# Kernel optimization log

Measured on AMD Instinct MI355X. Metric: run time of the kernel, lower is better.

## Reference

```python
import jax, jax.numpy as jnp
import numpy as np

B, N, K, H = 2, 2048, 48, 128
NIN = 2 * H          # num_in = 2*num_hidden (ProteinMPNN wiring)
FF = 4 * H           # PositionWiseFeedForward hidden
SCALE = 30.0
EPS = 1e-5           # torch LayerNorm default eps


def _ln(x, g, b):
    m = jnp.mean(x, axis=-1, keepdims=True)
    v = jnp.mean((x - m) ** 2, axis=-1, keepdims=True)
    return (x - m) / jnp.sqrt(v + EPS) * g + b


def _gelu(x):
    return jax.nn.gelu(x, approximate=False)  # torch.nn.GELU default (erf)


def _lin(x, W, b):
    return x @ W + b


def setup_inputs() -> dict:
    key = jax.random.key(0)
    ks = jax.random.split(key, 24)
    s = 0.05
    inp = {
        "h_V": jax.random.normal(ks[0], (B, N, H), jnp.float32),
        "h_E": jax.random.normal(ks[1], (B, N, K, H), jnp.float32),
        "E_idx": jax.random.randint(ks[2], (B, N, K), 0, N, jnp.int64),
        "mask_V": jnp.ones((B, N), jnp.float32),
        "mask_attend": jnp.ones((B, N, K), jnp.float32),
        # message MLP (node update): W1 in = H + NIN = 3H
        "W1": jax.random.normal(ks[3], (3 * H, H), jnp.float32) * s,
        "b1": jnp.zeros((H,), jnp.float32),
        "W2": jax.random.normal(ks[4], (H, H), jnp.float32) * s,
        "b2": jnp.zeros((H,), jnp.float32),
        "W3": jax.random.normal(ks[5], (H, H), jnp.float32) * s,
        "b3": jnp.zeros((H,), jnp.float32),
        # PositionWiseFeedForward
        "Wd_in": jax.random.normal(ks[6], (H, FF), jnp.float32) * s,
        "bd_in": jnp.zeros((FF,), jnp.float32),
        "Wd_out": jax.random.normal(ks[7], (FF, H), jnp.float32) * s,
        "bd_out": jnp.zeros((H,), jnp.float32),
        # edge-update MLP: W11 in = H + NIN = 3H
        "W11": jax.random.normal(ks[8], (3 * H, H), jnp.float32) * s,
        "b11": jnp.zeros((H,), jnp.float32),
        "W12": jax.random.normal(ks[9], (H, H), jnp.float32) * s,
        "b12": jnp.zeros((H,), jnp.float32),
        "W13": jax.random.normal(ks[10], (H, H), jnp.float32) * s,
        "b13": jnp.zeros((H,), jnp.float32),
        # LayerNorms
        "n1g": jnp.ones((H,), jnp.float32), "n1b": jnp.zeros((H,), jnp.float32),
        "n2g": jnp.ones((H,), jnp.float32), "n2b": jnp.zeros((H,), jnp.float32),
        "n3g": jnp.ones((H,), jnp.float32), "n3b": jnp.zeros((H,), jnp.float32),
    }
    return inp


def reference(h_V, h_E, E_idx, mask_V, mask_attend,
              W1, b1, W2, b2, W3, b3,
              Wd_in, bd_in, Wd_out, bd_out,
              W11, b11, W12, b12, W13, b13,
              n1g, n1b, n2g, n2b, n3g, n3b):
    gather = jax.vmap(lambda hv, idx: hv[idx])  # [B,N,H],[B,N,K] -> [B,N,K,H]

    # --- node update: cat_neighbors_nodes + expand + 3-layer GELU MLP ---
    h_nb = gather(h_V, E_idx)                                   # [B,N,K,H]
    hV_exp = jnp.broadcast_to(h_V[:, :, None, :], h_nb.shape)   # [B,N,K,H]
    h_EV = jnp.concatenate([hV_exp, h_E, h_nb], axis=-1)        # [B,N,K,3H]
    h_msg = _lin(_gelu(_lin(_gelu(_lin(h_EV, W1, b1)), W2, b2)), W3, b3)
    h_msg = mask_attend[..., None] * h_msg
    dh = jnp.sum(h_msg, axis=-2) / SCALE                        # masked-sum reduce
    h_V = _ln(h_V + dh, n1g, n1b)

    # --- position-wise FFN ---
    dh = _lin(_gelu(_lin(h_V, Wd_in, bd_in)), Wd_out, bd_out)
    h_V = _ln(h_V + dh, n2g, n2b)
    h_V = mask_V[..., None] * h_V

    # --- edge update (not last layer) ---
    h_nb2 = gather(h_V, E_idx)
    hV_exp2 = jnp.broadcast_to(h_V[:, :, None, :], h_nb2.shape)
    h_EV2 = jnp.concatenate([hV_exp2, h_E, h_nb2], axis=-1)     # [B,N,K,3H]
    h_msg2 = _lin(_gelu(_lin(_gelu(_lin(h_EV2, W11, b11)), W12, b12)), W13, b13)
    h_E = _ln(h_E + h_msg2, n3g, n3b)
    return (h_V, h_E)
```

## Files before the change

### kernel.cpp

```cpp
#include <hip/hip_runtime.h>
#include <hip/hip_bf16.h>
#include <stdint.h>

#define XP2 264
#define MP 136
#define FFP 520
#define EPIP 132

typedef __attribute__((ext_vector_type(8))) short bf16x8;
typedef __attribute__((ext_vector_type(4))) float f32x4;

__device__ __forceinline__ f32x4 mfma16(bf16x8 a, bf16x8 b, f32x4 c) {
  return __builtin_amdgcn_mfma_f32_16x16x32_bf16(a, b, c, 0, 0, 0);
}

__device__ __forceinline__ uint16_t f2b(float f) {
  union { __hip_bfloat16 h; uint16_t u; } v;
  v.h = __float2bfloat16(f);
  return v.u;
}
__device__ __forceinline__ uint32_t pk2f(float a, float b) {
  union { __hip_bfloat162 h; uint32_t u; } v;
  v.h = __float22bfloat162_rn(make_float2(a, b));
  return v.u;
}
__device__ __forceinline__ float gelu_f(float x) {
  float u = __builtin_fmaf(x * x, 0.044715f, 1.0f);
  float e = __builtin_amdgcn_exp2f(-2.302585093f * x * u);
  return x * __builtin_amdgcn_rcpf(1.0f + e);
}

__global__ __launch_bounds__(256) void k_prep(
    const float* __restrict__ hV,
    const float* __restrict__ W1, const float* __restrict__ W2, const float* __restrict__ W3,
    const float* __restrict__ WdIn, const float* __restrict__ WdOut,
    const float* __restrict__ W11, const float* __restrict__ W12, const float* __restrict__ W13,
    uint16_t* __restrict__ hVb,
    uint16_t* __restrict__ W1t, uint16_t* __restrict__ W2t, uint16_t* __restrict__ W3t,
    uint16_t* __restrict__ WdInT, uint16_t* __restrict__ WdOutT,
    uint16_t* __restrict__ W11t, uint16_t* __restrict__ W12t, uint16_t* __restrict__ W13t) {
  int i = blockIdx.x * 256 + threadIdx.x;
  if (i < 524288) { hVb[i] = f2b(hV[i]); return; }
  int j = i - 524288;
  if (j < 49152) { int n = j / 384, k = j - n * 384; W1t[j] = f2b(W1[k * 128 + n]); return; }
  j -= 49152;
  if (j < 16384) { int n = j >> 7, k = j & 127; W2t[j] = f2b(W2[k * 128 + n]); return; }
  j -= 16384;
  if (j < 16384) { int n = j >> 7, k = j & 127; W3t[j] = f2b(W3[k * 128 + n]); return; }
  j -= 16384;
  if (j < 65536) { int n = j >> 7, k = j & 127; WdInT[j] = f2b(WdIn[k * 512 + n]); return; }
  j -= 65536;
  if (j < 65536) { int n = j >> 9, k = j & 511; WdOutT[j] = f2b(WdOut[k * 128 + n]); return; }
  j -= 65536;
  if (j < 49152) { int n = j / 384, k = j - n * 384; W11t[j] = f2b(W11[k * 128 + n]); return; }
  j -= 49152;
  if (j < 16384) { int n = j >> 7, k = j & 127; W12t[j] = f2b(W12[k * 128 + n]); return; }
  j -= 16384;
  if (j < 16384) { int n = j >> 7, k = j & 127; W13t[j] = f2b(W13[k * 128 + n]); return; }
}

__global__ __launch_bounds__(256) void k_vec(
    const uint16_t* __restrict__ Xb, const uint16_t* __restrict__ Wt,
    const float* __restrict__ bias, float* __restrict__ C) {
  const int tid = threadIdx.x;
  const int lane = tid & 63, w = tid >> 6, l15 = lane & 15, lg = lane >> 4;
  const int row0 = blockIdx.x * 64 + w * 16;
  f32x4 acc[8] = {};
#pragma unroll
  for (int ks = 0; ks < 4; ++ks) {
    bf16x8 a = *(const bf16x8*)(Xb + (row0 + l15) * 128 + ks * 32 + lg * 8);
#pragma unroll
    for (int j = 0; j < 8; ++j) {
      bf16x8 bb = *(const bf16x8*)(Wt + (j * 16 + l15) * 384 + ks * 32 + lg * 8);
      acc[j] = mfma16(a, bb, acc[j]);
    }
  }
#pragma unroll
  for (int j = 0; j < 8; ++j) {
    float bs = bias[j * 16 + l15];
#pragma unroll
    for (int r = 0; r < 4; ++r)
      C[(row0 + lg * 4 + r) * 128 + j * 16 + l15] = acc[j][r] + bs;
  }
}

#define BUILD_XT(GSRC)                                                              \
  do {                                                                              \
    for (int idx = tid; idx < 48 * 32; idx += 256) {                                \
      int k_ = idx >> 5;                                                            \
      int c_ = idx & 31;                                                            \
      uint4 v_;                                                                     \
      if (c_ < 16) {                                                                \
        const float* s_ = hE + (size_t)(bn * 48 + k_) * 128 + (c_ << 3);            \
        float4 f0_ = *(const float4*)s_;                                            \
        float4 f1_ = *(const float4*)(s_ + 4);                                      \
        v_ = make_uint4(pk2f(f0_.x, f0_.y), pk2f(f0_.z, f0_.w),                     \
                        pk2f(f1_.x, f1_.y), pk2f(f1_.z, f1_.w));                    \
      } else {                                                                      \
        v_ = *(const uint4*)((GSRC) + (size_t)nbr[k_] * 128 + ((c_ - 16) << 3));    \
      }                                                                             \
      *(uint4*)(xt + k_ * XP2 + (c_ << 3)) = v_;                                    \
    }                                                                               \
  } while (0)

#define PRELOAD_W384(WT, WF)                                                        \
  do {                                                                              \
    const uint16_t* p0_ = (WT) + (w * 32 + l15) * 384 + 128 + lg * 8;               \
    const uint16_t* p1_ = p0_ + 16 * 384;                                           \
    _Pragma("unroll") for (int ks = 0; ks < 8; ++ks) {                              \
      WF[ks] = *(const bf16x8*)(p0_ + ks * 32);                                     \
      WF[8 + ks] = *(const bf16x8*)(p1_ + ks * 32);                                 \
    }                                                                               \
  } while (0)

#define PRELOAD_W128(WT, WF)                                                        \
  do {                                                                              \
    const uint16_t* p0_ = (WT) + (w * 32 + l15) * 128 + lg * 8;                     \
    const uint16_t* p1_ = p0_ + 16 * 128;                                           \
    _Pragma("unroll") for (int ks = 0; ks < 4; ++ks) {                              \
      WF[ks] = *(const bf16x8*)(p0_ + ks * 32);                                     \
      WF[4 + ks] = *(const bf16x8*)(p1_ + ks * 32);                                 \
    }                                                                               \
  } while (0)

#define LAYER256R(WF, ACC)                                                          \
  do {                                                                              \
    _Pragma("unroll") for (int ks = 0; ks < 8; ++ks)                                \
    _Pragma("unroll") for (int m = 0; m < 3; ++m) {                                 \
      bf16x8 a_ = *(const bf16x8*)(xt + (m * 16 + l15) * XP2 + ks * 32 + lg * 8);   \
      ACC[m][0] = mfma16(a_, WF[ks], ACC[m][0]);                                    \
      ACC[m][1] = mfma16(a_, WF[8 + ks], ACC[m][1]);                                \
    }                                                                               \
  } while (0)

#define LAYER128R(WF, ASRC, ACC)                                                    \
  do {                                                                              \
    _Pragma("unroll") for (int ks = 0; ks < 4; ++ks)                                \
    _Pragma("unroll") for (int m = 0; m < 3; ++m) {                                 \
      bf16x8 a_ = *(const bf16x8*)((ASRC) + (m * 16 + l15) * MP + ks * 32 + lg * 8);\
      ACC[m][0] = mfma16(a_, WF[ks], ACC[m][0]);                                    \
      ACC[m][1] = mfma16(a_, WF[4 + ks], ACC[m][1]);                                \
    }                                                                               \
  } while (0)

#define GSTORE(ACC, BIAS, DST)                                                      \
  do {                                                                              \
    float bA_ = (BIAS)[w * 32 + l15];                                               \
    float bB_ = (BIAS)[w * 32 + 16 + l15];                                          \
    _Pragma("unroll") for (int m = 0; m < 3; ++m)                                   \
    _Pragma("unroll") for (int r = 0; r < 4; ++r) {                                 \
      int row_ = m * 16 + lg * 4 + r;                                               \
      (DST)[row_ * MP + w * 32 + l15] = f2b(gelu_f(ACC[m][0][r] + bA_));            \
      (DST)[row_ * MP + w * 32 + 16 + l15] = f2b(gelu_f(ACC[m][1][r] + bB_));       \
    }                                                                               \
  } while (0)

#define GSTORE0(ACC, DST)                                                           \
  do {                                                                              \
    _Pragma("unroll") for (int m = 0; m < 3; ++m)                                   \
    _Pragma("unroll") for (int r = 0; r < 4; ++r) {                                 \
      int row_ = m * 16 + lg * 4 + r;                                               \
      (DST)[row_ * MP + w * 32 + l15] = f2b(gelu_f(ACC[m][0][r]));                  \
      (DST)[row_ * MP + w * 32 + 16 + l15] = f2b(gelu_f(ACC[m][1][r]));             \
    }                                                                               \
  } while (0)

#define ACC_INIT(ACC, CV)                                                           \
  do {                                                                              \
    float c0_ = (CV)[bn * 128 + w * 32 + l15];                                      \
    float c1_ = (CV)[bn * 128 + w * 32 + 16 + l15];                                 \
    _Pragma("unroll") for (int m = 0; m < 3; ++m) {                                 \
      ACC[m][0] = (f32x4){c0_, c0_, c0_, c0_};                                      \
      ACC[m][1] = (f32x4){c1_, c1_, c1_, c1_};                                      \
    }                                                                               \
  } while (0)

__global__ __launch_bounds__(256, 4) void k_node(
    const float* __restrict__ hV, const float* __restrict__ hE,
    const int* __restrict__ eidx, const float* __restrict__ maskA,
    const float* __restrict__ bias2, const float* __restrict__ bias3,
    const float* __restrict__ g1, const float* __restrict__ be1,
    const uint16_t* __restrict__ hVb, const float* __restrict__ C1,
    const uint16_t* __restrict__ W1t, const uint16_t* __restrict__ W2t,
    const uint16_t* __restrict__ W3t,
    float* __restrict__ hV1, uint16_t* __restrict__ hV1b) {
  __shared__ __align__(16) unsigned char lds[26880];
  uint16_t* xt = (uint16_t*)lds;
  uint16_t* midA = (uint16_t*)lds;
  uint16_t* midB = (uint16_t*)(lds + 13056);
  int* nbr = (int*)(lds + 26112);
  float* dh = (float*)(lds + 26368);

  const int tid = threadIdx.x;
  const int lane = tid & 63;
  const int w = tid >> 6;
  const int l15 = lane & 15;
  const int lg = lane >> 4;
  const int bn = blockIdx.x;
  const int b = bn >> 11;

  bf16x8 w1f[16];
  PRELOAD_W384(W1t, w1f);

  if (tid < 48) nbr[tid] = (b << 11) + eidx[bn * 48 + tid];
  __syncthreads();

  BUILD_XT(hVb);
  __syncthreads();

  f32x4 acc1[3][2];
  ACC_INIT(acc1, C1);
  LAYER256R(w1f, acc1);
  bf16x8 w2f[8];
  PRELOAD_W128(W2t, w2f);
  __syncthreads();
  GSTORE0(acc1, midA);
  __syncthreads();

  f32x4 acc2[3][2] = {};
  LAYER128R(w2f, midA, acc2);
  bf16x8 w3f[8];
  PRELOAD_W128(W3t, w3f);
  GSTORE(acc2, bias2, midB);
  __syncthreads();

  f32x4 acc3[3][2] = {};
  LAYER128R(w3f, midB, acc3);

  {
    float bA = bias3[w * 32 + l15];
    float bB = bias3[w * 32 + 16 + l15];
    float s0 = 0.f, s1 = 0.f;
#pragma unroll
    for (int m = 0; m < 3; ++m)
#pragma unroll
      for (int r = 0; r < 4; ++r) {
        int row = m * 16 + lg * 4 + r;
        float mk = maskA[bn * 48 + row];
        s0 += (acc3[m][0][r] + bA) * mk;
        s1 += (acc3[m][1][r] + bB) * mk;
      }
    s0 += __shfl_xor(s0, 16); s0 += __shfl_xor(s0, 32);
    s1 += __shfl_xor(s1, 16); s1 += __shfl_xor(s1, 32);
    if (lg == 0) { dh[w * 32 + l15] = s0; dh[w * 32 + 16 + l15] = s1; }
  }
  __syncthreads();

  if (w == 0) {
    const float inv = 1.0f / 30.0f;
    float x0 = hV[bn * 128 + lane] + dh[lane] * inv;
    float x1 = hV[bn * 128 + 64 + lane] + dh[64 + lane] * inv;
    float s = x0 + x1, q = x0 * x0 + x1 * x1;
#pragma unroll
    for (int off = 1; off < 64; off <<= 1) {
      s += __shfl_xor(s, off);
      q += __shfl_xor(q, off);
    }
    float mean = s * (1.0f / 128.0f);
    float var = q * (1.0f / 128.0f) - mean * mean;
    float rstd = rsqrtf(var + 1e-5f);
    float y0 = (x0 - mean) * rstd * g1[lane] + be1[lane];
    float y1 = (x1 - mean) * rstd * g1[64 + lane] + be1[64 + lane];
    hV1[bn * 128 + lane] = y0;
    hV1[bn * 128 + 64 + lane] = y1;
    hV1b[bn * 128 + lane] = f2b(y0);
    hV1b[bn * 128 + 64 + lane] = f2b(y1);
  }
}

__global__ __launch_bounds__(256, 2) void k_ffn(
    const float* __restrict__ hV1, const uint16_t* __restrict__ hV1b,
    const float* __restrict__ maskV,
    const float* __restrict__ bdin, const float* __restrict__ bdout,
    const float* __restrict__ g2, const float* __restrict__ be2,
    const uint16_t* __restrict__ WdInT, const uint16_t* __restrict__ WdOutT,
    float* __restrict__ outV, uint16_t* __restrict__ hV2b) {
  __shared__ __align__(16) unsigned char lds[20992];
  uint16_t* xa = (uint16_t*)lds;
  uint16_t* mf = (uint16_t*)(lds + 4352);
  float* epi = (float*)(lds + 4352);

  const int tid = threadIdx.x;
  const int lane = tid & 63;
  const int w = tid >> 6;
  const int l15 = lane & 15;
  const int lg = lane >> 4;
  const int node0 = blockIdx.x * 16;

  {
    int row = tid >> 4, c = tid & 15;
    *(uint4*)(xa + row * 136 + (c << 3)) =
        *(const uint4*)(hV1b + (node0 + row) * 128 + (c << 3));
  }
  __syncthreads();

  f32x4 acc[8] = {};
  {
    const uint16_t* ar = xa + l15 * 136 + lg * 8;
#pragma unroll
    for (int ks = 0; ks < 4; ++ks) {
      bf16x8 a = *(const bf16x8*)(ar + ks * 32);
#pragma unroll
      for (int j = 0; j < 8; ++j) {
        bf16x8 bb = *(const bf16x8*)(WdInT + ((w * 8 + j) * 16 + l15) * 128 + ks * 32 + lg * 8);
        acc[j] = mfma16(a, bb, acc[j]);
      }
    }
  }
#pragma unroll
  for (int j = 0; j < 8; ++j) {
    int col = (w * 8 + j) * 16 + l15;
    float bs = bdin[col];
#pragma unroll
    for (int r = 0; r < 4; ++r) {
      int row = lg * 4 + r;
      mf[row * FFP + col] = f2b(gelu_f(acc[j][r] + bs));
    }
  }
  __syncthreads();

  f32x4 acc2[2] = {};
  {
    const uint16_t* mr = mf + l15 * FFP + lg * 8;
#pragma unroll 4
    for (int ks = 0; ks < 16; ++ks) {
      bf16x8 a = *(const bf16x8*)(mr + ks * 32);
#pragma unroll
      for (int t = 0; t < 2; ++t) {
        bf16x8 bb = *(const bf16x8*)(WdOutT + ((w * 2 + t) * 16 + l15) * 512 + ks * 32 + lg * 8);
        acc2[t] = mfma16(a, bb, acc2[t]);
      }
    }
  }
  __syncthreads();
#pragma unroll
  for (int t = 0; t < 2; ++t) {
    int col = (w * 2 + t) * 16 + l15;
    float bs = bdout[col];
#pragma unroll
    for (int r = 0; r < 4; ++r) {
      int row = lg * 4 + r;
      epi[row * EPIP + col] = acc2[t][r] + bs;
    }
  }
  __syncthreads();

#pragma unroll
  for (int rr = 0; rr < 4; ++rr) {
    int row = w * 4 + rr;
    int node = node0 + row;
    float x0 = epi[row * EPIP + lane] + hV1[node * 128 + lane];
    float x1 = epi[row * EPIP + 64 + lane] + hV1[node * 128 + 64 + lane];
    float s = x0 + x1, q = x0 * x0 + x1 * x1;
#pragma unroll
    for (int off = 1; off < 64; off <<= 1) {
      s += __shfl_xor(s, off);
      q += __shfl_xor(q, off);
    }
    float mean = s * (1.0f / 128.0f);
    float var = q * (1.0f / 128.0f) - mean * mean;
    float rstd = rsqrtf(var + 1e-5f);
    float mv = maskV[node];
    float y0 = mv * ((x0 - mean) * rstd * g2[lane] + be2[lane]);
    float y1 = mv * ((x1 - mean) * rstd * g2[64 + lane] + be2[64 + lane]);
    outV[node * 128 + lane] = y0;
    outV[node * 128 + 64 + lane] = y1;
    hV2b[node * 128 + lane] = f2b(y0);
    hV2b[node * 128 + 64 + lane] = f2b(y1);
  }
}

__global__ __launch_bounds__(256, 4) void k_edge(
    const float* __restrict__ hE, const int* __restrict__ eidx,
    const float* __restrict__ bias2, const float* __restrict__ bias3,
    const float* __restrict__ g3, const float* __restrict__ be3,
    const uint16_t* __restrict__ hV2b, const float* __restrict__ C2,
    const uint16_t* __restrict__ W1t, const uint16_t* __restrict__ W2t,
    const uint16_t* __restrict__ W3t,
    float* __restrict__ outE) {
  __shared__ __align__(16) unsigned char lds[26304];
  uint16_t* xt = (uint16_t*)lds;
  uint16_t* midA = (uint16_t*)lds;
  uint16_t* midB = (uint16_t*)(lds + 13056);
  int* nbr = (int*)(lds + 26112);
  float* part_s = (float*)lds;
  float* part_q = (float*)(lds + 768);
  float* mstd = (float*)(lds + 1536);

  const int tid = threadIdx.x;
  const int lane = tid & 63;
  const int w = tid >> 6;
  const int l15 = lane & 15;
  const int lg = lane >> 4;
  const int bn = blockIdx.x;
  const int b = bn >> 11;

  bf16x8 w1f[16];
  PRELOAD_W384(W1t, w1f);

  if (tid < 48) nbr[tid] = (b << 11) + eidx[bn * 48 + tid];
  __syncthreads();

  BUILD_XT(hV2b);
  __syncthreads();

  f32x4 acc1[3][2];
  ACC_INIT(acc1, C2);
  LAYER256R(w1f, acc1);
  bf16x8 w2f[8];
  PRELOAD_W128(W2t, w2f);
  __syncthreads();
  GSTORE0(acc1, midA);
  __syncthreads();

  f32x4 acc2[3][2] = {};
  LAYER128R(w2f, midA, acc2);
  bf16x8 w3f[8];
  PRELOAD_W128(W3t, w3f);
  GSTORE(acc2, bias2, midB);
  __syncthreads();

  f32x4 acc3[3][2] = {};
  LAYER128R(w3f, midB, acc3);

  const float bA = bias3[w * 32 + l15];
  const float bB = bias3[w * 32 + 16 + l15];

  float xs0[3][4], xs1[3][4];
#pragma unroll
  for (int m = 0; m < 3; ++m)
#pragma unroll
    for (int r = 0; r < 4; ++r) {
      int row = m * 16 + lg * 4 + r;
      size_t e = (size_t)bn * 48 + row;
      xs0[m][r] = acc3[m][0][r] + bA + hE[e * 128 + w * 32 + l15];
      xs1[m][r] = acc3[m][1][r] + bB + hE[e * 128 + w * 32 + 16 + l15];
      float s = xs0[m][r] + xs1[m][r];
      float q = xs0[m][r] * xs0[m][r] + xs1[m][r] * xs1[m][r];
      s += __shfl_xor(s, 1); q += __shfl_xor(q, 1);
      s += __shfl_xor(s, 2); q += __shfl_xor(q, 2);
      s += __shfl_xor(s, 4); q += __shfl_xor(q, 4);
      s += __shfl_xor(s, 8); q += __shfl_xor(q, 8);
      if (l15 == 0) { part_s[row * 4 + w] = s; part_q[row * 4 + w] = q; }
    }
  __syncthreads();

  if (tid < 48) {
    float s = part_s[tid * 4] + part_s[tid * 4 + 1] + part_s[tid * 4 + 2] + part_s[tid * 4 + 3];
    float q = part_q[tid * 4] + part_q[tid * 4 + 1] + part_q[tid * 4 + 2] + part_q[tid * 4 + 3];
    float mean = s * (1.0f / 128.0f);
    float var = q * (1.0f / 128.0f) - mean * mean;
    mstd[tid * 2] = mean;
    mstd[tid * 2 + 1] = rsqrtf(var + 1e-5f);
  }
  __syncthreads();

  const float gA = g3[w * 32 + l15], beA = be3[w * 32 + l15];
  const float gB = g3[w * 32 + 16 + l15], beB = be3[w * 32 + 16 + l15];
#pragma unroll
  for (int m = 0; m < 3; ++m)
#pragma unroll
    for (int r = 0; r < 4; ++r) {
      int row = m * 16 + lg * 4 + r;
      size_t e = (size_t)bn * 48 + row;
      float mean = mstd[row * 2];
      float rstd = mstd[row * 2 + 1];
      outE[e * 128 + w * 32 + l15] = (xs0[m][r] - mean) * rstd * gA + beA;
      outE[e * 128 + w * 32 + 16 + l15] = (xs1[m][r] - mean) * rstd * gB + beB;
    }
}

extern "C" void kernel_launch(void* const* d_in, const int* in_sizes, int n_in,
                              void* d_out, int out_size, void* d_ws, size_t ws_size,
                              hipStream_t stream) {
  const float* hV = (const float*)d_in[0];
  const float* hE = (const float*)d_in[1];
  const int* eidx = (const int*)d_in[2];
  const float* maskV = (const float*)d_in[3];
  const float* maskA = (const float*)d_in[4];
  const float* W1 = (const float*)d_in[5];   const float* b1 = (const float*)d_in[6];
  const float* W2 = (const float*)d_in[7];   const float* b2 = (const float*)d_in[8];
  const float* W3 = (const float*)d_in[9];   const float* b3 = (const float*)d_in[10];
  const float* WdIn = (const float*)d_in[11];  const float* bdin = (const float*)d_in[12];
  const float* WdOut = (const float*)d_in[13]; const float* bdout = (const float*)d_in[14];
  const float* W11 = (const float*)d_in[15]; const float* b11 = (const float*)d_in[16];
  const float* W12 = (const float*)d_in[17]; const float* b12 = (const float*)d_in[18];
  const float* W13 = (const float*)d_in[19]; const float* b13 = (const float*)d_in[20];
  const float* n1g = (const float*)d_in[21]; const float* n1b = (const float*)d_in[22];
  const float* n2g = (const float*)d_in[23]; const float* n2b = (const float*)d_in[24];
  const float* n3g = (const float*)d_in[25]; const float* n3b = (const float*)d_in[26];

  char* ws = (char*)d_ws;
  uint16_t* hVb    = (uint16_t*)(ws + 0);
  uint16_t* W1t    = (uint16_t*)(ws + 1048576);
  uint16_t* W2t    = (uint16_t*)(ws + 1146880);
  uint16_t* W3t    = (uint16_t*)(ws + 1179648);
  uint16_t* WdInT  = (uint16_t*)(ws + 1212416);
  uint16_t* WdOutT = (uint16_t*)(ws + 1343488);
  uint16_t* W11t   = (uint16_t*)(ws + 1474560);
  uint16_t* W12t   = (uint16_t*)(ws + 1572864);
  uint16_t* W13t   = (uint16_t*)(ws + 1605632);
  float*    hV1    = (float*)(ws + 1638400);
  uint16_t* hV1b   = (uint16_t*)(ws + 3735552);
  uint16_t* hV2b   = (uint16_t*)(ws + 4784128);
  float*    C1     = (float*)(ws + 5832704);
  float*    C2     = (float*)(ws + 7929856);

  float* outV = (float*)d_out;
  float* outE = (float*)d_out + 524288;

  k_prep<<<3200, 256, 0, stream>>>(hV, W1, W2, W3, WdIn, WdOut, W11, W12, W13,
                                   hVb, W1t, W2t, W3t, WdInT, WdOutT, W11t, W12t, W13t);
  k_vec<<<64, 256, 0, stream>>>(hVb, W1t, b1, C1);
  k_node<<<4096, 256, 0, stream>>>(hV, hE, eidx, maskA, b2, b3, n1g, n1b,
                                   hVb, C1, W1t, W2t, W3t, hV1, hV1b);
  k_ffn<<<256, 256, 0, stream>>>(hV1, hV1b, maskV, bdin, bdout, n2g, n2b,
                                 WdInT, WdOutT, outV, hV2b);
  k_vec<<<64, 256, 0, stream>>>(hV2b, W11t, b11, C2);
  k_edge<<<4096, 256, 0, stream>>>(hE, eidx, b12, b13, n3g, n3b,
                                   hV2b, C2, W11t, W12t, W13t, outE);
}
```

Baseline: 224.6 us.

## Process two nodes per block in node and edge MLP kernels

The k_node and k_edge kernels now handle 96 edge rows (two nodes) per block instead of 48. Launch count is halved and LDS staging is doubled. This amortizes the register-resident weight preload (W1/W2/W3 fragments) and the per-block setup over twice the MFMA work. The cost is doubled accumulator registers and LDS per block, with launch bounds dropped from 4 to 3 waves per SIMD, which lowers occupancy and latency hiding.

```diff
diff --git a/kernel.cpp b/kernel.cpp
--- a/kernel.cpp
+++ b/kernel.cpp
@@ -84,14 +84,14 @@
   }
 }
 
-#define BUILD_XT(GSRC)                                                              \
-  do {                                                                              \
-    for (int idx = tid; idx < 48 * 32; idx += 256) {                                \
+#define BUILD_XT96(GSRC)                                                            \
+  do {                                                                              \
+    for (int idx = tid; idx < 96 * 32; idx += 256) {                                \
       int k_ = idx >> 5;                                                            \
       int c_ = idx & 31;                                                            \
       uint4 v_;                                                                     \
       if (c_ < 16) {                                                                \
-        const float* s_ = hE + (size_t)(bn * 48 + k_) * 128 + (c_ << 3);            \
+        const float* s_ = hE + (size_t)(base + k_) * 128 + (c_ << 3);               \
         float4 f0_ = *(const float4*)s_;                                            \
         float4 f1_ = *(const float4*)(s_ + 4);                                      \
         v_ = make_uint4(pk2f(f0_.x, f0_.y), pk2f(f0_.z, f0_.w),                     \
@@ -123,31 +123,31 @@
     }                                                                               \
   } while (0)
 
-#define LAYER256R(WF, ACC)                                                          \
+#define LAYER256R6(WF, ACC)                                                         \
   do {                                                                              \
     _Pragma("unroll") for (int ks = 0; ks < 8; ++ks)                                \
-    _Pragma("unroll") for (int m = 0; m < 3; ++m) {                                 \
+    _Pragma("unroll") for (int m = 0; m < 6; ++m) {                                 \
       bf16x8 a_ = *(const bf16x8*)(xt + (m * 16 + l15) * XP2 + ks * 32 + lg * 8);   \
       ACC[m][0] = mfma16(a_, WF[ks], ACC[m][0]);                                    \
       ACC[m][1] = mfma16(a_, WF[8 + ks], ACC[m][1]);                                \
     }                                                                               \
   } while (0)
 
-#define LAYER128R(WF, ASRC, ACC)                                                    \
+#define LAYER128R6(WF, ASRC, ACC)                                                   \
   do {                                                                              \
     _Pragma("unroll") for (int ks = 0; ks < 4; ++ks)                                \
-    _Pragma("unroll") for (int m = 0; m < 3; ++m) {                                 \
+    _Pragma("unroll") for (int m = 0; m < 6; ++m) {                                 \
       bf16x8 a_ = *(const bf16x8*)((ASRC) + (m * 16 + l15) * MP + ks * 32 + lg * 8);\
       ACC[m][0] = mfma16(a_, WF[ks], ACC[m][0]);                                    \
       ACC[m][1] = mfma16(a_, WF[4 + ks], ACC[m][1]);                                \
     }                                                                               \
   } while (0)
 
-#define GSTORE(ACC, BIAS, DST)                                                      \
+#define GSTORE6(ACC, BIAS, DST)                                                     \
   do {                                                                              \
     float bA_ = (BIAS)[w * 32 + l15];                                               \
     float bB_ = (BIAS)[w * 32 + 16 + l15];                                          \
-    _Pragma("unroll") for (int m = 0; m < 3; ++m)                                   \
+    _Pragma("unroll") for (int m = 0; m < 6; ++m)                                   \
     _Pragma("unroll") for (int r = 0; r < 4; ++r) {                                 \
       int row_ = m * 16 + lg * 4 + r;                                               \
       (DST)[row_ * MP + w * 32 + l15] = f2b(gelu_f(ACC[m][0][r] + bA_));            \
@@ -155,9 +155,9 @@
     }                                                                               \
   } while (0)
 
-#define GSTORE0(ACC, DST)                                                           \
-  do {                                                                              \
-    _Pragma("unroll") for (int m = 0; m < 3; ++m)                                   \
+#define GSTORE06(ACC, DST)                                                          \
+  do {                                                                              \
+    _Pragma("unroll") for (int m = 0; m < 6; ++m)                                   \
     _Pragma("unroll") for (int r = 0; r < 4; ++r) {                                 \
       int row_ = m * 16 + lg * 4 + r;                                               \
       (DST)[row_ * MP + w * 32 + l15] = f2b(gelu_f(ACC[m][0][r]));                  \
@@ -165,17 +165,21 @@
     }                                                                               \
   } while (0)
 
-#define ACC_INIT(ACC, CV)                                                           \
-  do {                                                                              \
-    float c0_ = (CV)[bn * 128 + w * 32 + l15];                                      \
-    float c1_ = (CV)[bn * 128 + w * 32 + 16 + l15];                                 \
-    _Pragma("unroll") for (int m = 0; m < 3; ++m) {                                 \
-      ACC[m][0] = (f32x4){c0_, c0_, c0_, c0_};                                      \
-      ACC[m][1] = (f32x4){c1_, c1_, c1_, c1_};                                      \
-    }                                                                               \
-  } while (0)
-
-__global__ __launch_bounds__(256, 4) void k_node(
+#define ACC_INIT6(ACC, CV)                                                          \
+  do {                                                                              \
+    float c0a_ = (CV)[(size_t)nd0 * 128 + w * 32 + l15];                            \
+    float c1a_ = (CV)[(size_t)nd0 * 128 + w * 32 + 16 + l15];                       \
+    float c0b_ = (CV)[(size_t)(nd0 + 1) * 128 + w * 32 + l15];                      \
+    float c1b_ = (CV)[(size_t)(nd0 + 1) * 128 + w * 32 + 16 + l15];                 \
+    _Pragma("unroll") for (int m = 0; m < 6; ++m) {                                 \
+      float a_ = (m < 3) ? c0a_ : c0b_;                                             \
+      float b_ = (m < 3) ? c1a_ : c1b_;                                             \
+      ACC[m][0] = (f32x4){a_, a_, a_, a_};                                          \
+      ACC[m][1] = (f32x4){b_, b_, b_, b_};                                          \
+    }                                                                               \
+  } while (0)
+
+__global__ __launch_bounds__(256, 3) void k_node(
     const float* __restrict__ hV, const float* __restrict__ hE,
     const int* __restrict__ eidx, const float* __restrict__ maskA,
     const float* __restrict__ bias2, const float* __restrict__ bias3,
@@ -184,72 +188,82 @@
     const uint16_t* __restrict__ W1t, const uint16_t* __restrict__ W2t,
     const uint16_t* __restrict__ W3t,
     float* __restrict__ hV1, uint16_t* __restrict__ hV1b) {
-  __shared__ __align__(16) unsigned char lds[26880];
+  __shared__ __align__(16) unsigned char lds[52608];
   uint16_t* xt = (uint16_t*)lds;
   uint16_t* midA = (uint16_t*)lds;
-  uint16_t* midB = (uint16_t*)(lds + 13056);
-  int* nbr = (int*)(lds + 26112);
-  float* dh = (float*)(lds + 26368);
+  uint16_t* midB = (uint16_t*)(lds + 26112);
+  int* nbr = (int*)(lds + 52224);
+  float* dh = (float*)lds;
 
   const int tid = threadIdx.x;
   const int lane = tid & 63;
   const int w = tid >> 6;
   const int l15 = lane & 15;
   const int lg = lane >> 4;
-  const int bn = blockIdx.x;
-  const int b = bn >> 11;
+  const int nd0 = blockIdx.x * 2;
+  const int base = blockIdx.x * 96;
 
   bf16x8 w1f[16];
   PRELOAD_W384(W1t, w1f);
 
-  if (tid < 48) nbr[tid] = (b << 11) + eidx[bn * 48 + tid];
-  __syncthreads();
-
-  BUILD_XT(hVb);
-  __syncthreads();
-
-  f32x4 acc1[3][2];
-  ACC_INIT(acc1, C1);
-  LAYER256R(w1f, acc1);
+  if (tid < 96) {
+    int e = base + tid;
+    nbr[tid] = ((e >= 98304) ? 2048 : 0) + eidx[e];
+  }
+  __syncthreads();
+
+  BUILD_XT96(hVb);
+  __syncthreads();
+
+  f32x4 acc1[6][2];
+  ACC_INIT6(acc1, C1);
+  LAYER256R6(w1f, acc1);
   bf16x8 w2f[8];
   PRELOAD_W128(W2t, w2f);
   __syncthreads();
-  GSTORE0(acc1, midA);
-  __syncthreads();
-
-  f32x4 acc2[3][2] = {};
-  LAYER128R(w2f, midA, acc2);
+  GSTORE06(acc1, midA);
+  __syncthreads();
+
+  f32x4 acc2[6][2] = {};
+  LAYER128R6(w2f, midA, acc2);
   bf16x8 w3f[8];
   PRELOAD_W128(W3t, w3f);
-  GSTORE(acc2, bias2, midB);
-  __syncthreads();
-
-  f32x4 acc3[3][2] = {};
-  LAYER128R(w3f, midB, acc3);
+  GSTORE6(acc2, bias2, midB);
+  __syncthreads();
+
+  f32x4 acc3[6][2] = {};
+  LAYER128R6(w3f, midB, acc3);
 
   {
     float bA = bias3[w * 32 + l15];
     float bB = bias3[w * 32 + 16 + l15];
-    float s0 = 0.f, s1 = 0.f;
-#pragma unroll
-    for (int m = 0; m < 3; ++m)
+    float s0a = 0.f, s1a = 0.f, s0b = 0.f, s1b = 0.f;
+#pragma unroll
+    for (int m = 0; m < 6; ++m)
 #pragma unroll
       for (int r = 0; r < 4; ++r) {
         int row = m * 16 + lg * 4 + r;
-        float mk = maskA[bn * 48 + row];
-        s0 += (acc3[m][0][r] + bA) * mk;
-        s1 += (acc3[m][1][r] + bB) * mk;
+        float mk = maskA[base + row];
+        float v0 = (acc3[m][0][r] + bA) * mk;
+        float v1 = (acc3[m][1][r] + bB) * mk;
+        if (m < 3) { s0a += v0; s1a += v1; } else { s0b += v0; s1b += v1; }
       }
-    s0 += __shfl_xor(s0, 16); s0 += __shfl_xor(s0, 32);
-    s1 += __shfl_xor(s1, 16); s1 += __shfl_xor(s1, 32);
-    if (lg == 0) { dh[w * 32 + l15] = s0; dh[w * 32 + 16 + l15] = s1; }
-  }
-  __syncthreads();
-
-  if (w == 0) {
+    s0a += __shfl_xor(s0a, 16); s0a += __shfl_xor(s0a, 32);
+    s1a += __shfl_xor(s1a, 16); s1a += __shfl_xor(s1a, 32);
+    s0b += __shfl_xor(s0b, 16); s0b += __shfl_xor(s0b, 32);
+    s1b += __shfl_xor(s1b, 16); s1b += __shfl_xor(s1b, 32);
+    if (lg == 0) {
+      dh[w * 32 + l15] = s0a;        dh[w * 32 + 16 + l15] = s1a;
+      dh[128 + w * 32 + l15] = s0b;  dh[128 + w * 32 + 16 + l15] = s1b;
+    }
+  }
+  __syncthreads();
+
+  if (w < 2) {
+    int node = nd0 + w;
     const float inv = 1.0f / 30.0f;
-    float x0 = hV[bn * 128 + lane] + dh[lane] * inv;
-    float x1 = hV[bn * 128 + 64 + lane] + dh[64 + lane] * inv;
+    float x0 = hV[(size_t)node * 128 + lane] + dh[w * 128 + lane] * inv;
+    float x1 = hV[(size_t)node * 128 + 64 + lane] + dh[w * 128 + 64 + lane] * inv;
     float s = x0 + x1, q = x0 * x0 + x1 * x1;
 #pragma unroll
     for (int off = 1; off < 64; off <<= 1) {
@@ -261,10 +275,10 @@
     float rstd = rsqrtf(var + 1e-5f);
     float y0 = (x0 - mean) * rstd * g1[lane] + be1[lane];
     float y1 = (x1 - mean) * rstd * g1[64 + lane] + be1[64 + lane];
-    hV1[bn * 128 + lane] = y0;
-    hV1[bn * 128 + 64 + lane] = y1;
-    hV1b[bn * 128 + lane] = f2b(y0);
-    hV1b[bn * 128 + 64 + lane] = f2b(y1);
+    hV1[(size_t)node * 128 + lane] = y0;
+    hV1[(size_t)node * 128 + 64 + lane] = y1;
+    hV1b[(size_t)node * 128 + lane] = f2b(y0);
+    hV1b[(size_t)node * 128 + 64 + lane] = f2b(y1);
   }
 }
 
@@ -370,7 +384,7 @@
   }
 }
 
-__global__ __launch_bounds__(256, 4) void k_edge(
+__global__ __launch_bounds__(256, 3) void k_edge(
     const float* __restrict__ hE, const int* __restrict__ eidx,
     const float* __restrict__ bias2, const float* __restrict__ bias3,
     const float* __restrict__ g3, const float* __restrict__ be3,
@@ -378,61 +392,64 @@
     const uint16_t* __restrict__ W1t, const uint16_t* __restrict__ W2t,
     const uint16_t* __restrict__ W3t,
     float* __restrict__ outE) {
-  __shared__ __align__(16) unsigned char lds[26304];
+  __shared__ __align__(16) unsigned char lds[52608];
   uint16_t* xt = (uint16_t*)lds;
   uint16_t* midA = (uint16_t*)lds;
-  uint16_t* midB = (uint16_t*)(lds + 13056);
-  int* nbr = (int*)(lds + 26112);
+  uint16_t* midB = (uint16_t*)(lds + 26112);
+  int* nbr = (int*)(lds + 52224);
   float* part_s = (float*)lds;
-  float* part_q = (float*)(lds + 768);
-  float* mstd = (float*)(lds + 1536);
+  float* part_q = (float*)(lds + 1536);
+  float* mstd = (float*)(lds + 3072);
 
   const int tid = threadIdx.x;
   const int lane = tid & 63;
   const int w = tid >> 6;
   const int l15 = lane & 15;
   const int lg = lane >> 4;
-  const int bn = blockIdx.x;
-  const int b = bn >> 11;
+  const int nd0 = blockIdx.x * 2;
+  const int base = blockIdx.x * 96;
 
   bf16x8 w1f[16];
   PRELOAD_W384(W1t, w1f);
 
-  if (tid < 48) nbr[tid] = (b << 11) + eidx[bn * 48 + tid];
-  __syncthreads();
-
-  BUILD_XT(hV2b);
-  __syncthreads();
-
-  f32x4 acc1[3][2];
-  ACC_INIT(acc1, C2);
-  LAYER256R(w1f, acc1);
+  if (tid < 96) {
+    int e = base + tid;
+    nbr[tid] = ((e >= 98304) ? 2048 : 0) + eidx[e];
+  }
+  __syncthreads();
+
+  BUILD_XT96(hV2b);
+  __syncthreads();
+
+  f32x4 acc1[6][2];
+  ACC_INIT6(acc1, C2);
+  LAYER256R6(w1f, acc1);
   bf16x8 w2f[8];
   PRELOAD_W128(W2t, w2f);
   __syncthreads();
-  GSTORE0(acc1, midA);
-  __syncthreads();
-
-  f32x4 acc2[3][2] = {};
-  LAYER128R(w2f, midA, acc2);
+  GSTORE06(acc1, midA);
+  __syncthreads();
+
+  f32x4 acc2[6][2] = {};
+  LAYER128R6(w2f, midA, acc2);
   bf16x8 w3f[8];
   PRELOAD_W128(W3t, w3f);
-  GSTORE(acc2, bias2, midB);
-  __syncthreads();
-
-  f32x4 acc3[3][2] = {};
-  LAYER128R(w3f, midB, acc3);
+  GSTORE6(acc2, bias2, midB);
+  __syncthreads();
+
+  f32x4 acc3[6][2] = {};
+  LAYER128R6(w3f, midB, acc3);
 
   const float bA = bias3[w * 32 + l15];
   const float bB = bias3[w * 32 + 16 + l15];
 
-  float xs0[3][4], xs1[3][4];
-#pragma unroll
-  for (int m = 0; m < 3; ++m)
+  float xs0[6][4], xs1[6][4];
+#pragma unroll
+  for (int m = 0; m < 6; ++m)
 #pragma unroll
     for (int r = 0; r < 4; ++r) {
       int row = m * 16 + lg * 4 + r;
-      size_t e = (size_t)bn * 48 + row;
+      size_t e = (size_t)base + row;
       xs0[m][r] = acc3[m][0][r] + bA + hE[e * 128 + w * 32 + l15];
       xs1[m][r] = acc3[m][1][r] + bB + hE[e * 128 + w * 32 + 16 + l15];
       float s = xs0[m][r] + xs1[m][r];
@@ -445,7 +462,7 @@
     }
   __syncthreads();
 
-  if (tid < 48) {
+  if (tid < 96) {
     float s = part_s[tid * 4] + part_s[tid * 4 + 1] + part_s[tid * 4 + 2] + part_s[tid * 4 + 3];
     float q = part_q[tid * 4] + part_q[tid * 4 + 1] + part_q[tid * 4 + 2] + part_q[tid * 4 + 3];
     float mean = s * (1.0f / 128.0f);
@@ -458,11 +475,11 @@
   const float gA = g3[w * 32 + l15], beA = be3[w * 32 + l15];
   const float gB = g3[w * 32 + 16 + l15], beB = be3[w * 32 + 16 + l15];
 #pragma unroll
-  for (int m = 0; m < 3; ++m)
+  for (int m = 0; m < 6; ++m)
 #pragma unroll
     for (int r = 0; r < 4; ++r) {
       int row = m * 16 + lg * 4 + r;
-      size_t e = (size_t)bn * 48 + row;
+      size_t e = (size_t)base + row;
       float mean = mstd[row * 2];
       float rstd = mstd[row * 2 + 1];
       outE[e * 128 + w * 32 + l15] = (xs0[m][r] - mean) * rstd * gA + beA;
@@ -512,11 +529,11 @@
   k_prep<<<3200, 256, 0, stream>>>(hV, W1, W2, W3, WdIn, WdOut, W11, W12, W13,
                                    hVb, W1t, W2t, W3t, WdInT, WdOutT, W11t, W12t, W13t);
   k_vec<<<64, 256, 0, stream>>>(hVb, W1t, b1, C1);
-  k_node<<<4096, 256, 0, stream>>>(hV, hE, eidx, maskA, b2, b3, n1g, n1b,
+  k_node<<<2048, 256, 0, stream>>>(hV, hE, eidx, maskA, b2, b3, n1g, n1b,
                                    hVb, C1, W1t, W2t, W3t, hV1, hV1b);
   k_ffn<<<256, 256, 0, stream>>>(hV1, hV1b, maskV, bdin, bdout, n2g, n2b,
                                  WdInT, WdOutT, outV, hV2b);
   k_vec<<<64, 256, 0, stream>>>(hV2b, W11t, b11, C2);
-  k_edge<<<4096, 256, 0, stream>>>(hE, eidx, b12, b13, n3g, n3b,
+  k_edge<<<2048, 256, 0, stream>>>(hE, eidx, b12, b13, n3g, n3b,
                                    hV2b, C2, W11t, W12t, W13t, outE);
 }
```

Result: no change. 222.1 us (-1.1%).
